# Performance work log

Measured on AMD Instinct MI355X. Metric: run time of the kernel, lower is better.

## Reference

```python
import jax, jax.numpy as jnp
import numpy as np

B, L, H, D = 2, 2048, 16, 64
E = H * D  # 1024

def setup_inputs() -> dict:
    key = jax.random.key(0)
    k1, k2, k3 = jax.random.split(key, 3)
    net_in = jax.random.normal(k1, (B, L, E), dtype=jnp.float32)
    # torch nn.Linear weights are [out_features, in_features]; scale like kaiming-uniform-ish
    W_qkv = jax.random.normal(k2, (3 * E, E), dtype=jnp.float32) * (1.0 / np.sqrt(E))
    W_out = jax.random.normal(k3, (E, E), dtype=jnp.float32) * (1.0 / np.sqrt(E))
    return {"net_in": net_in, "W_qkv": W_qkv, "W_out": W_out}

def reference(net_in, W_qkv, W_out):
    b, l, c = net_in.shape
    h, d = H, D
    # c_proj: x @ W_qkv.T -> (B, L, 3E), split into q, k, v
    qkv = jnp.einsum('blc,ec->ble', net_in, W_qkv)
    q, k, v = jnp.split(qkv, 3, axis=-1)
    # reshape to (B, H, L, D)
    q = q.reshape(b, l, h, d).transpose(0, 2, 1, 3)
    k = k.reshape(b, l, h, d).transpose(0, 2, 1, 3)
    v = v.reshape(b, l, h, d).transpose(0, 2, 1, 3)
    scale = 1.0 / np.sqrt(d).astype(np.float32)
    attn = jnp.einsum('bhqd,bhkd->bhqk', q, k) * scale  # (B, H, L, L)
    causal = jnp.tril(jnp.ones((l, l), dtype=bool))
    attn = jnp.where(causal[None, None, :, :], attn, -jnp.inf)
    attn = jax.nn.softmax(attn, axis=-1)
    out = jnp.einsum('bhqk,bhkd->bhqd', attn, v)  # (B, H, L, D)
    out = out.transpose(0, 2, 1, 3).reshape(b, l, c)
    return jnp.einsum('blc,ec->ble', out, W_out)
```

## Files before the change

kernel.cpp:

```cpp
#include <hip/hip_runtime.h>
#include <hip/hip_bf16.h>

#define LOG2E 1.44269504088896340736f

typedef __attribute__((ext_vector_type(8))) short s16x8;
typedef __attribute__((ext_vector_type(4))) short s16x4;
typedef __attribute__((ext_vector_type(2))) unsigned int u32x2;
typedef __attribute__((ext_vector_type(4))) float f32x4;
typedef __attribute__((ext_vector_type(16))) float f32x16;

__device__ inline short f2bf(float f) {
  __hip_bfloat16 h = __float2bfloat16(f);
  union { __hip_bfloat16 h; short s; } u; u.h = h; return u.s;
}

__device__ inline void gl_lds16(const void* g, void* l) {
  __builtin_amdgcn_global_load_lds(
      (const __attribute__((address_space(1))) void*)g,
      (__attribute__((address_space(3))) void*)l, 16, 0, 0);
}

__global__ __launch_bounds__(256)
void cvt_all(const float* __restrict__ Wqkv, const float* __restrict__ Wout,
             const float* __restrict__ net,
             short* __restrict__ dWqkv, short* __restrict__ dWout,
             short* __restrict__ dnet) {
  int bid = blockIdx.x;
  const float* src; short* dst; int i;
  if (bid < 3072)      { src = Wqkv; dst = dWqkv; i = bid * 256 + threadIdx.x; }
  else if (bid < 4096) { src = Wout; dst = dWout; i = (bid - 3072) * 256 + threadIdx.x; }
  else                 { src = net;  dst = dnet;  i = (bid - 4096) * 256 + threadIdx.x; }
  f32x4 v = ((const f32x4*)src)[i];
  s16x4 o;
  o[0] = f2bf(v[0]); o[1] = f2bf(v[1]); o[2] = f2bf(v[2]); o[3] = f2bf(v[3]);
  ((s16x4*)dst)[i] = o;
}

template<int OUTF32, int VTRANS, int SPLITK, int NSUB>
__global__ __launch_bounds__(256)
void gemm128(const short* __restrict__ A, int lda,
             const short* __restrict__ B, int ldb,
             void* __restrict__ Cp, int ldc, int Klen,
             short* __restrict__ P1) {
  int id = (int)(blockIdx.x + (blockIdx.y << 5));
  int xcd = id & 7, slot = id >> 3;
  int m0 = (slot & 31) * 128;
  int n0 = (xcd * NSUB + (slot >> 5)) * 128;
  int kbeg = SPLITK ? (int)blockIdx.z * Klen : 0;
  int t = threadIdx.x;
  int w = t >> 6, lane = t & 63;
  int l16 = lane & 15, quad = lane >> 4;
  int wm = w >> 1, wn = w & 1;

  __shared__ __align__(16) short As[2][128 * 32];
  __shared__ __align__(16) short Bs[2][128 * 32];

  int scell = ((t & 3) ^ ((t >> 3) & 3)) * 8;
  const short* bsrc = B + (size_t)(n0 + (t >> 2)) * ldb + kbeg + scell;
  const short* asrc = A + (size_t)(m0 + (t >> 2)) * lda + kbeg + scell;
  int rcell = (quad ^ ((l16 >> 1) & 3)) * 8;

  f32x4 acc[4][4];
#pragma unroll
  for (int i = 0; i < 4; ++i)
#pragma unroll
    for (int j = 0; j < 4; ++j) acc[i][j] = (f32x4){0.f, 0.f, 0.f, 0.f};

#pragma unroll
  for (int r = 0; r < 2; ++r) {
    gl_lds16(asrc + (size_t)r * 64 * lda, (char*)As + r * 4096 + w * 1024);
    gl_lds16(bsrc + (size_t)r * 64 * ldb, (char*)Bs + r * 4096 + w * 1024);
  }
  __syncthreads();

  int nks = Klen >> 5;
  for (int ks = 0; ks < nks; ++ks) {
    int cur = ks & 1;
    if (ks + 1 < nks) {
      int k0 = (ks + 1) * 32;
      int nb = cur ^ 1;
#pragma unroll
      for (int r = 0; r < 2; ++r) {
        gl_lds16(asrc + k0 + (size_t)r * 64 * lda, (char*)As + nb * 8192 + r * 4096 + w * 1024);
        gl_lds16(bsrc + k0 + (size_t)r * 64 * ldb, (char*)Bs + nb * 8192 + r * 4096 + w * 1024);
      }
    }

    s16x8 af[4], bf[4];
#pragma unroll
    for (int i = 0; i < 4; ++i) {
      af[i] = *(const s16x8*)(As[cur] + (wm * 64 + i * 16 + l16) * 32 + rcell);
      bf[i] = *(const s16x8*)(Bs[cur] + (wn * 64 + i * 16 + l16) * 32 + rcell);
    }
#pragma unroll
    for (int i = 0; i < 4; ++i)
#pragma unroll
      for (int j = 0; j < 4; ++j)
        acc[i][j] = __builtin_amdgcn_mfma_f32_16x16x32_bf16(af[i], bf[j], acc[i][j], 0, 0, 0);

    __syncthreads();
  }

  if (SPLITK && blockIdx.z == 1) {
#pragma unroll
    for (int i = 0; i < 4; ++i)
#pragma unroll
      for (int j = 0; j < 4; ++j)
#pragma unroll
        for (int rr = 0; rr < 4; ++rr) {
          size_t row = m0 + wm * 64 + i * 16 + quad * 4 + rr;
          size_t col = n0 + wn * 64 + j * 16 + l16;
          float* fp = (float*)(P1 + row * 3072 + 1024);
          fp[col] = acc[i][j][rr];
        }
  } else if (VTRANS && n0 >= 2048) {
    short* Cs = (short*)Cp;
#pragma unroll
    for (int i = 0; i < 4; ++i)
#pragma unroll
      for (int j = 0; j < 4; ++j) {
        int colg = n0 + wn * 64 + j * 16 + l16;
        int d = colg & 63;
        size_t dst = (size_t)(m0 + wm * 64 + d) * ldc + (colg - d) + i * 16 + quad * 4;
        s16x4 ob;
#pragma unroll
        for (int rr = 0; rr < 4; ++rr) ob[rr] = f2bf(acc[i][j][rr]);
        *(s16x4*)(Cs + dst) = ob;
      }
  } else {
#pragma unroll
    for (int i = 0; i < 4; ++i)
#pragma unroll
      for (int j = 0; j < 4; ++j)
#pragma unroll
        for (int rr = 0; rr < 4; ++rr) {
          size_t row = m0 + wm * 64 + i * 16 + quad * 4 + rr;
          size_t col = n0 + wn * 64 + j * 16 + l16;
          if (OUTF32) ((float*)Cp)[row * ldc + col] = acc[i][j][rr];
          else        ((short*)Cp)[row * ldc + col] = f2bf(acc[i][j][rr]);
        }
  }
}

__global__ __launch_bounds__(256)
void reduce_add(float* __restrict__ out, const short* __restrict__ qkv) {
  int row = blockIdx.x;
  int c = threadIdx.x;
  const f32x4* p = (const f32x4*)(qkv + (size_t)row * 3072 + 1024);
  f32x4* o = (f32x4*)(out + (size_t)row * 1024);
  f32x4 v = o[c];
  f32x4 q = p[c];
  v[0] += q[0]; v[1] += q[1]; v[2] += q[2]; v[3] += q[3];
  o[c] = v;
}

__global__ __launch_bounds__(256, 4)
void attn(short* __restrict__ qkv) {
  const int L = 2048, E3 = 3072, EO = 1024;
  int id = (int)(blockIdx.x + (blockIdx.y << 5));
  int xcd = id & 7;
  int s = id >> 3;
  int bh = xcd * 4 + (s & 3);
  int u = s >> 2;
  int vv = u & 15;
  int qidx = (u & 16) ? (31 - vv) : vv;
  int b = bh >> 4, h = bh & 15;
  int q0 = qidx * 64;
  int t = threadIdx.x;
  int wave = t >> 6, lane = t & 63;
  int qh = wave >> 1, kh = wave & 1;
  int l31 = lane & 31, hsel = lane >> 5;
  int khi4 = hsel * 4;
  int key = (lane >> 1) & 3;
  const float SENT = -3.0e38f;
  const float SC = 0.125f * LOG2E;

  __shared__ __align__(16) short Ks[2][2][64][32];
  __shared__ __align__(16) short Vt[2][2][64][32];

  int rowbase = b * L;

  s16x8 qf[4];
  {
    const short* qp = qkv + (size_t)(rowbase + q0 + qh * 32 + l31) * E3 + h * 64 + hsel * 8;
#pragma unroll
    for (int e = 0; e < 4; ++e) {
      s16x8 raw = *(const s16x8*)(qp + e * 16);
#pragma unroll
      for (int j = 0; j < 8; ++j) {
        union { float f; int i; } u2; u2.i = ((int)(unsigned short)raw[j]) << 16;
        raw[j] = f2bf(u2.f * SC);
      }
      qf[e] = raw;
    }
  }

  int scell = ((lane & 3) ^ ((lane >> 3) & 3)) * 8;
  const short* ksrc = qkv + (size_t)(rowbase + wave * 16 + (lane >> 2)) * E3 + EO
                      + h * 64 + scell;
  const short* vsrc = qkv + (size_t)(rowbase + wave * 16 + (lane >> 2)) * E3 + 2 * EO
                      + h * 64 + scell;

  float l_acc = 0.f;
  f32x16 o0 = (f32x16){0.f,0.f,0.f,0.f,0.f,0.f,0.f,0.f,0.f,0.f,0.f,0.f,0.f,0.f,0.f,0.f};
  f32x16 o1 = o0;

  int nkb = qidx + 1;

  gl_lds16(ksrc,      (char*)Ks + wave * 1024);
  gl_lds16(ksrc + 32, (char*)Ks + 4096 + wave * 1024);
  gl_lds16(vsrc,      (char*)Vt + wave * 1024);
  gl_lds16(vsrc + 32, (char*)Vt + 4096 + wave * 1024);

  for (int kb = 0; kb < nkb; ++kb) {
    int cur = kb & 1;
    __syncthreads();
    if (kb + 1 < nkb) {
      size_t koff = (size_t)((kb + 1) * 64) * E3;
      int nb = cur ^ 1;
      gl_lds16(ksrc + koff,      (char*)Ks + nb * 8192 + wave * 1024);
      gl_lds16(ksrc + koff + 32, (char*)Ks + nb * 8192 + 4096 + wave * 1024);
      gl_lds16(vsrc + koff,      (char*)Vt + nb * 8192 + wave * 1024);
      gl_lds16(vsrc + koff + 32, (char*)Vt + nb * 8192 + 4096 + wave * 1024);
    }

    int rel = (q0 + qh * 32) - (kb * 64 + kh * 32);
    if (rel > -32) {
      int krow = kh * 32 + l31;
      s16x8 kf0 = *(const s16x8*)(&Ks[cur][0][krow][((0 + hsel) ^ key) * 8]);
      s16x8 kf1 = *(const s16x8*)(&Ks[cur][0][krow][((2 + hsel) ^ key) * 8]);
      s16x8 kf2 = *(const s16x8*)(&Ks[cur][1][krow][((0 + hsel) ^ key) * 8]);
      s16x8 kf3 = *(const s16x8*)(&Ks[cur][1][krow][((2 + hsel) ^ key) * 8]);
      s16x8 vf00 = *(const s16x8*)(&Vt[cur][kh][ 0 + l31][((0 + hsel) ^ key) * 8]);
      s16x8 vf01 = *(const s16x8*)(&Vt[cur][kh][32 + l31][((0 + hsel) ^ key) * 8]);
      s16x8 vf10 = *(const s16x8*)(&Vt[cur][kh][ 0 + l31][((2 + hsel) ^ key) * 8]);
      s16x8 vf11 = *(const s16x8*)(&Vt[cur][kh][32 + l31][((2 + hsel) ^ key) * 8]);

      f32x16 sf = (f32x16){0.f,0.f,0.f,0.f,0.f,0.f,0.f,0.f,0.f,0.f,0.f,0.f,0.f,0.f,0.f,0.f};
      sf = __builtin_amdgcn_mfma_f32_32x32x16_bf16(kf0, qf[0], sf, 0, 0, 0);
      sf = __builtin_amdgcn_mfma_f32_32x32x16_bf16(kf1, qf[1], sf, 0, 0, 0);
      sf = __builtin_amdgcn_mfma_f32_32x32x16_bf16(kf2, qf[2], sf, 0, 0, 0);
      sf = __builtin_amdgcn_mfma_f32_32x32x16_bf16(kf3, qf[3], sf, 0, 0, 0);

      if (rel < 31) {
        int thr = rel + l31 - khi4;
#pragma unroll
        for (int r = 0; r < 16; ++r) {
          const int base_k = (r & 3) + 8 * (r >> 2);
          if (base_k > thr) sf[r] = SENT;
        }
      }

      float pv[16];
#pragma unroll
      for (int r = 0; r < 16; ++r) {
        pv[r] = __builtin_amdgcn_exp2f(sf[r]);
        l_acc += pv[r];
      }

#define PKW(lo, hi) __builtin_amdgcn_perm(__float_as_uint(hi) + 0x8000u, \
                                          __float_as_uint(lo) + 0x8000u, 0x07060302u)
      unsigned A0 = PKW(pv[0],  pv[1]),  A1 = PKW(pv[2],  pv[3]);
      unsigned B0 = PKW(pv[4],  pv[5]),  B1 = PKW(pv[6],  pv[7]);
      unsigned C0 = PKW(pv[8],  pv[9]),  C1 = PKW(pv[10], pv[11]);
      unsigned D0 = PKW(pv[12], pv[13]), D1 = PKW(pv[14], pv[15]);
#undef PKW
      u32x2 sw0 = __builtin_amdgcn_permlane32_swap(A0, B0, false, false);
      u32x2 sw1 = __builtin_amdgcn_permlane32_swap(A1, B1, false, false);
      u32x2 sw2 = __builtin_amdgcn_permlane32_swap(C0, D0, false, false);
      u32x2 sw3 = __builtin_amdgcn_permlane32_swap(C1, D1, false, false);
      union { s16x8 v; unsigned u[4]; } P0, P1;
      P0.u[0] = sw0[0]; P0.u[1] = sw1[0]; P0.u[2] = sw0[1]; P0.u[3] = sw1[1];
      P1.u[0] = sw2[0]; P1.u[1] = sw3[0]; P1.u[2] = sw2[1]; P1.u[3] = sw3[1];

      o0 = __builtin_amdgcn_mfma_f32_32x32x16_bf16(vf00, P0.v, o0, 0, 0, 0);
      o0 = __builtin_amdgcn_mfma_f32_32x32x16_bf16(vf10, P1.v, o0, 0, 0, 0);
      o1 = __builtin_amdgcn_mfma_f32_32x32x16_bf16(vf01, P0.v, o1, 0, 0, 0);
      o1 = __builtin_amdgcn_mfma_f32_32x32x16_bf16(vf11, P1.v, o1, 0, 0, 0);
    }
  }

  l_acc += __shfl_xor(l_acc, 32);
  __syncthreads();
  float* fs = (float*)&Ks[0][0][0][0];
  float* lb = (float*)&Vt[0][0][0][0];
  if (kh) {
#pragma unroll
    for (int r = 0; r < 16; ++r) {
      fs[qh * 2048 + r * 64 + lane] = o0[r];
      fs[qh * 2048 + (16 + r) * 64 + lane] = o1[r];
    }
    if (lane < 32) lb[qh * 32 + lane] = l_acc;
  }
  __syncthreads();
  if (!kh) {
    float inv = 1.f / (l_acc + lb[qh * 32 + l31]);
    size_t obase = (size_t)(rowbase + q0 + qh * 32 + l31) * E3 + h * 64;
    int fb = qh * 2048;
#pragma unroll
    for (int g = 0; g < 4; ++g) {
      s16x4 w0, w1;
#pragma unroll
      for (int rr = 0; rr < 4; ++rr) {
        int r = g * 4 + rr;
        w0[rr] = f2bf((o0[r] + fs[fb + r * 64 + lane]) * inv);
        w1[rr] = f2bf((o1[r] + fs[fb + (16 + r) * 64 + lane]) * inv);
      }
      *(s16x4*)(qkv + obase + g * 8 + khi4) = w0;
      *(s16x4*)(qkv + obase + 32 + g * 8 + khi4) = w1;
    }
  }
}

extern "C" void kernel_launch(void* const* d_in, const int* in_sizes, int n_in,
                              void* d_out, int out_size, void* d_ws, size_t ws_size,
                              hipStream_t stream) {
  const float* net_in = (const float*)d_in[0];
  const float* W_qkv  = (const float*)d_in[1];
  const float* W_out  = (const float*)d_in[2];

  short* Wqkvb = (short*)d_ws;
  short* Woutb = Wqkvb + (size_t)3072 * 1024;
  short* qkv   = Woutb + (size_t)1024 * 1024;
  short* netb  = (short*)d_out;

  cvt_all<<<8192, 256, 0, stream>>>(W_qkv, W_out, net_in, Wqkvb, Woutb, netb);

  gemm128<0, 1, 0, 3><<<dim3(32, 24), 256, 0, stream>>>(netb, 1024, Wqkvb, 1024,
                                                        qkv, 3072, 1024, nullptr);
  attn<<<dim3(32, 32), 256, 0, stream>>>(qkv);
  gemm128<1, 0, 1, 1><<<dim3(32, 8, 2), 256, 0, stream>>>(qkv, 3072, Woutb, 1024,
                                                          d_out, 1024, 512, qkv);
  reduce_add<<<4096, 256, 0, stream>>>((float*)d_out, qkv);
}
```

Measured before the change: 171.8 us.

## Replace split-K output GEMM and reduce with 64x128-tile GEMM; use hardware bf16 pack

The output projection used to be a 128x128-tile split-K GEMM whose second half wrote fp32 partials into scratch, followed by a separate reduce kernel. It is now a dedicated 64x128-tile GEMM over the full K with 512 blocks, which removes the partial-sum traffic and one launch while keeping the same parallelism. The attention P packing also switches from manual round-and-perm to the v_cvt_pk_bf16_f32 instruction, which reduces VALU work and changes rounding to round-to-nearest-even.

```diff
diff --git a/kernel.cpp b/kernel.cpp
--- a/kernel.cpp
+++ b/kernel.cpp
@@ -12,6 +12,12 @@
 __device__ inline short f2bf(float f) {
   __hip_bfloat16 h = __float2bfloat16(f);
   union { __hip_bfloat16 h; short s; } u; u.h = h; return u.s;
+}
+
+__device__ inline unsigned cvtpk(float lo, float hi) {
+  unsigned r;
+  asm("v_cvt_pk_bf16_f32 %0, %1, %2" : "=v"(r) : "v"(lo), "v"(hi));
+  return r;
 }
 
 __device__ inline void gl_lds16(const void* g, void* l) {
@@ -36,17 +42,15 @@
   ((s16x4*)dst)[i] = o;
 }
 
-template<int OUTF32, int VTRANS, int SPLITK, int NSUB>
+template<int OUTF32, int VTRANS, int NSUB>
 __global__ __launch_bounds__(256)
 void gemm128(const short* __restrict__ A, int lda,
              const short* __restrict__ B, int ldb,
-             void* __restrict__ Cp, int ldc, int Klen,
-             short* __restrict__ P1) {
+             void* __restrict__ Cp, int ldc, int K) {
   int id = (int)(blockIdx.x + (blockIdx.y << 5));
   int xcd = id & 7, slot = id >> 3;
   int m0 = (slot & 31) * 128;
   int n0 = (xcd * NSUB + (slot >> 5)) * 128;
-  int kbeg = SPLITK ? (int)blockIdx.z * Klen : 0;
   int t = threadIdx.x;
   int w = t >> 6, lane = t & 63;
   int l16 = lane & 15, quad = lane >> 4;
@@ -56,8 +60,8 @@
   __shared__ __align__(16) short Bs[2][128 * 32];
 
   int scell = ((t & 3) ^ ((t >> 3) & 3)) * 8;
-  const short* bsrc = B + (size_t)(n0 + (t >> 2)) * ldb + kbeg + scell;
-  const short* asrc = A + (size_t)(m0 + (t >> 2)) * lda + kbeg + scell;
+  const short* bsrc = B + (size_t)(n0 + (t >> 2)) * ldb + scell;
+  const short* asrc = A + (size_t)(m0 + (t >> 2)) * lda + scell;
   int rcell = (quad ^ ((l16 >> 1) & 3)) * 8;
 
   f32x4 acc[4][4];
@@ -73,7 +77,7 @@
   }
   __syncthreads();
 
-  int nks = Klen >> 5;
+  int nks = K >> 5;
   for (int ks = 0; ks < nks; ++ks) {
     int cur = ks & 1;
     if (ks + 1 < nks) {
@@ -101,19 +105,7 @@
     __syncthreads();
   }
 
-  if (SPLITK && blockIdx.z == 1) {
-#pragma unroll
-    for (int i = 0; i < 4; ++i)
-#pragma unroll
-      for (int j = 0; j < 4; ++j)
-#pragma unroll
-        for (int rr = 0; rr < 4; ++rr) {
-          size_t row = m0 + wm * 64 + i * 16 + quad * 4 + rr;
-          size_t col = n0 + wn * 64 + j * 16 + l16;
-          float* fp = (float*)(P1 + row * 3072 + 1024);
-          fp[col] = acc[i][j][rr];
-        }
-  } else if (VTRANS && n0 >= 2048) {
+  if (VTRANS && n0 >= 2048) {
     short* Cs = (short*)Cp;
 #pragma unroll
     for (int i = 0; i < 4; ++i)
@@ -143,15 +135,76 @@
 }
 
 __global__ __launch_bounds__(256)
-void reduce_add(float* __restrict__ out, const short* __restrict__ qkv) {
-  int row = blockIdx.x;
-  int c = threadIdx.x;
-  const f32x4* p = (const f32x4*)(qkv + (size_t)row * 3072 + 1024);
-  f32x4* o = (f32x4*)(out + (size_t)row * 1024);
-  f32x4 v = o[c];
-  f32x4 q = p[c];
-  v[0] += q[0]; v[1] += q[1]; v[2] += q[2]; v[3] += q[3];
-  o[c] = v;
+void gemm64(const short* __restrict__ A, int lda,
+            const short* __restrict__ B, int ldb,
+            float* __restrict__ C, int ldc, int K) {
+  int id = (int)(blockIdx.x + (blockIdx.y << 5));
+  int xcd = id & 7, slot = id >> 3;
+  int m0 = slot * 64;
+  int n0 = xcd * 128;
+  int t = threadIdx.x;
+  int w = t >> 6, lane = t & 63;
+  int l16 = lane & 15, quad = lane >> 4;
+  int wm = w & 1, wn = w >> 1;
+
+  __shared__ __align__(16) short As[2][64 * 32];
+  __shared__ __align__(16) short Bs[2][128 * 32];
+
+  int scell = ((t & 3) ^ ((t >> 3) & 3)) * 8;
+  const short* asrc = A + (size_t)(m0 + (t >> 2)) * lda + scell;
+  const short* bsrc = B + (size_t)(n0 + (t >> 2)) * ldb + scell;
+  int rcell = (quad ^ ((l16 >> 1) & 3)) * 8;
+
+  f32x4 acc[2][4];
+#pragma unroll
+  for (int i = 0; i < 2; ++i)
+#pragma unroll
+    for (int j = 0; j < 4; ++j) acc[i][j] = (f32x4){0.f, 0.f, 0.f, 0.f};
+
+  gl_lds16(asrc, (char*)As + w * 1024);
+#pragma unroll
+  for (int r = 0; r < 2; ++r)
+    gl_lds16(bsrc + (size_t)r * 64 * ldb, (char*)Bs + r * 4096 + w * 1024);
+  __syncthreads();
+
+  int nks = K >> 5;
+  for (int ks = 0; ks < nks; ++ks) {
+    int cur = ks & 1;
+    if (ks + 1 < nks) {
+      int k0 = (ks + 1) * 32;
+      int nb = cur ^ 1;
+      gl_lds16(asrc + k0, (char*)As + nb * 4096 + w * 1024);
+#pragma unroll
+      for (int r = 0; r < 2; ++r)
+        gl_lds16(bsrc + k0 + (size_t)r * 64 * ldb, (char*)Bs + nb * 8192 + r * 4096 + w * 1024);
+    }
+
+    s16x8 af[2], bf[4];
+#pragma unroll
+    for (int i = 0; i < 2; ++i)
+      af[i] = *(const s16x8*)(As[cur] + (wm * 32 + i * 16 + l16) * 32 + rcell);
+#pragma unroll
+    for (int j = 0; j < 4; ++j)
+      bf[j] = *(const s16x8*)(Bs[cur] + (wn * 64 + j * 16 + l16) * 32 + rcell);
+#pragma unroll
+    for (int i = 0; i < 2; ++i)
+#pragma unroll
+      for (int j = 0; j < 4; ++j)
+        acc[i][j] = __builtin_amdgcn_mfma_f32_16x16x32_bf16(af[i], bf[j], acc[i][j], 0, 0, 0);
+
+    __syncthreads();
+  }
+
+#pragma unroll
+  for (int i = 0; i < 2; ++i)
+#pragma unroll
+    for (int j = 0; j < 4; ++j)
+#pragma unroll
+      for (int rr = 0; rr < 4; ++rr) {
+        size_t row = m0 + wm * 32 + i * 16 + quad * 4 + rr;
+        size_t col = n0 + wn * 64 + j * 16 + l16;
+        C[row * ldc + col] = acc[i][j][rr];
+      }
 }
 
 __global__ __launch_bounds__(256, 4)
@@ -258,13 +311,10 @@
         l_acc += pv[r];
       }
 
-#define PKW(lo, hi) __builtin_amdgcn_perm(__float_as_uint(hi) + 0x8000u, \
-                                          __float_as_uint(lo) + 0x8000u, 0x07060302u)
-      unsigned A0 = PKW(pv[0],  pv[1]),  A1 = PKW(pv[2],  pv[3]);
-      unsigned B0 = PKW(pv[4],  pv[5]),  B1 = PKW(pv[6],  pv[7]);
-      unsigned C0 = PKW(pv[8],  pv[9]),  C1 = PKW(pv[10], pv[11]);
-      unsigned D0 = PKW(pv[12], pv[13]), D1 = PKW(pv[14], pv[15]);
-#undef PKW
+      unsigned A0 = cvtpk(pv[0],  pv[1]),  A1 = cvtpk(pv[2],  pv[3]);
+      unsigned B0 = cvtpk(pv[4],  pv[5]),  B1 = cvtpk(pv[6],  pv[7]);
+      unsigned C0 = cvtpk(pv[8],  pv[9]),  C1 = cvtpk(pv[10], pv[11]);
+      unsigned D0 = cvtpk(pv[12], pv[13]), D1 = cvtpk(pv[14], pv[15]);
       u32x2 sw0 = __builtin_amdgcn_permlane32_swap(A0, B0, false, false);
       u32x2 sw1 = __builtin_amdgcn_permlane32_swap(A1, B1, false, false);
       u32x2 sw2 = __builtin_amdgcn_permlane32_swap(C0, D0, false, false);
@@ -326,10 +376,9 @@
 
   cvt_all<<<8192, 256, 0, stream>>>(W_qkv, W_out, net_in, Wqkvb, Woutb, netb);
 
-  gemm128<0, 1, 0, 3><<<dim3(32, 24), 256, 0, stream>>>(netb, 1024, Wqkvb, 1024,
-                                                        qkv, 3072, 1024, nullptr);
+  gemm128<0, 1, 3><<<dim3(32, 24), 256, 0, stream>>>(netb, 1024, Wqkvb, 1024,
+                                                     qkv, 3072, 1024);
   attn<<<dim3(32, 32), 256, 0, stream>>>(qkv);
-  gemm128<1, 0, 1, 1><<<dim3(32, 8, 2), 256, 0, stream>>>(qkv, 3072, Woutb, 1024,
-                                                          d_out, 1024, 512, qkv);
-  reduce_add<<<4096, 256, 0, stream>>>((float*)d_out, qkv);
-}
+  gemm64<<<dim3(32, 16), 256, 0, stream>>>(qkv, 3072, Woutb, 1024,
+                                           (float*)d_out, 1024, 1024);
+}
```

Result: faster. 165.0 us (-4.0%).
